# Optimization experiments

Hardware: AMD Instinct MI355X
Metric: run time of the kernel (lower is better)

## Reference

```python
import jax, jax.numpy as jnp
import numpy as np

EPS_SIGMA = 1e-6
EPS_NORM = 1e-6


def _filters(mu_x, mu_y, sigma_x, sigma_y, W, H):
    # squash params as in forward(): tanh for means, sigmoid for sigmas
    mu_x = jnp.tanh(mu_x)
    mu_y = jnp.tanh(mu_y)
    sx = jnp.exp(1.5 - 2.0 * jax.nn.sigmoid(sigma_x))  # [N]
    sy = jnp.exp(1.5 - 2.0 * jax.nn.sigmoid(sigma_y))
    # Sigma is diagonal, so its inverse is elementwise reciprocal
    inv_x = 1.0 / (sx ** 2 + EPS_SIGMA)  # [N]
    inv_y = 1.0 / (sy ** 2 + EPS_SIGMA)
    mux = (W - 1) * ((mu_x + 1.0) / 2.0)  # [N], pixel-space mean along width
    muy = (H - 1) * ((mu_y + 1.0) / 2.0)
    xs = jnp.arange(W, dtype=jnp.float32)
    ys = jnp.arange(H, dtype=jnp.float32)
    dx = xs[None, :, None] - mux[:, None, None]  # [N,W,1]
    dy = ys[None, None, :] - muy[:, None, None]  # [N,1,H]
    quad = dx ** 2 * inv_x[:, None, None] + dy ** 2 * inv_y[:, None, None]  # [N,W,H]
    f = jnp.exp(-0.5 * quad)
    return f / (jnp.sum(f, axis=(1, 2), keepdims=True) + EPS_NORM)  # [N,W,H]


def setup_inputs() -> dict:
    key = jax.random.key(0)
    k1, k2, k3, k4, k5 = jax.random.split(key, 5)
    B, C, T, W, H, N = 8, 1024, 64, 14, 14, 3
    video = jax.random.normal(k1, (B, C, T, W, H), dtype=jnp.float32)
    mu_x = 0.5 * jax.random.normal(k2, (N,), dtype=jnp.float32)
    mu_y = 0.5 * jax.random.normal(k3, (N,), dtype=jnp.float32)
    sigma_x = 1e-4 * jax.random.normal(k4, (N,), dtype=jnp.float32)
    sigma_y = 1e-4 * jax.random.normal(k5, (N,), dtype=jnp.float32)
    return {"video": video, "mu_x": mu_x, "mu_y": mu_y,
            "sigma_x": sigma_x, "sigma_y": sigma_y}


def reference(video, mu_x, mu_y, sigma_x, sigma_y):
    B, C, T, W, H = video.shape
    f = _filters(mu_x, mu_y, sigma_x, sigma_y, W, H)  # [N,W,H]
    N = f.shape[0]
    # weighted spatial sum, then mean over time; avoids the Ni-repeated video
    o = jnp.einsum('bctwh,nwh->bcn', video, f) / T  # [B,C,N]
    return o.reshape(B, C * N)
```

## Files before the change

kernel.cpp:

```cpp
#include <hip/hip_runtime.h>
#include <math.h>

#define B_  8
#define C_  1024
#define T_  64
#define W_  14
#define H_  14
#define N_  3
#define WH  (W_ * H_)
#define WH4 (WH / 4)

__global__ void attn_pool_kernel(const float* __restrict__ video,
                                 const float* __restrict__ mu_x,
                                 const float* __restrict__ mu_y,
                                 const float* __restrict__ sigma_x,
                                 const float* __restrict__ sigma_y,
                                 float* __restrict__ out)
{
    const int wave = threadIdx.x >> 6;
    const int lane = threadIdx.x & 63;
    const int bc   = blockIdx.x * 4 + wave;

    float fv[N_][4];
#pragma unroll
    for (int n = 0; n < N_; ++n)
#pragma unroll
        for (int j = 0; j < 4; ++j) fv[n][j] = 0.0f;

    if (lane < WH4) {
#pragma unroll
        for (int n = 0; n < N_; ++n) {
            const float mux  = 6.5f * (tanhf(mu_x[n]) + 1.0f);
            const float muy  = 6.5f * (tanhf(mu_y[n]) + 1.0f);
            const float sgx  = 1.0f / (1.0f + expf(-sigma_x[n]));
            const float sgy  = 1.0f / (1.0f + expf(-sigma_y[n]));
            const float invx = 1.0f / (expf(3.0f - 4.0f * sgx) + 1e-6f);
            const float invy = 1.0f / (expf(3.0f - 4.0f * sgy) + 1e-6f);
#pragma unroll
            for (int j = 0; j < 4; ++j) {
                const int   wh = 4 * lane + j;
                const int   w  = wh / H_;
                const int   h  = wh - w * H_;
                const float dx = (float)w - mux;
                const float dy = (float)h - muy;
                fv[n][j] = expf(-0.5f * (dx * dx * invx + dy * dy * invy));
            }
        }
    }
#pragma unroll
    for (int n = 0; n < N_; ++n) {
        float s = fv[n][0] + fv[n][1] + fv[n][2] + fv[n][3];
#pragma unroll
        for (int off = 32; off > 0; off >>= 1) s += __shfl_xor(s, off);
        const float norm = 1.0f / (s + 1e-6f);
#pragma unroll
        for (int j = 0; j < 4; ++j) fv[n][j] *= norm;
    }

    const float4* v4 = (const float4*)(video + (size_t)bc * (size_t)(T_ * WH));
    float a0 = 0.0f, a1 = 0.0f, a2 = 0.0f;
    if (lane < WH4) {
#pragma unroll 8
        for (int t = 0; t < T_; ++t) {
            const float4 v = v4[t * WH4 + lane];
            a0 += v.x * fv[0][0] + v.y * fv[0][1] + v.z * fv[0][2] + v.w * fv[0][3];
            a1 += v.x * fv[1][0] + v.y * fv[1][1] + v.z * fv[1][2] + v.w * fv[1][3];
            a2 += v.x * fv[2][0] + v.y * fv[2][1] + v.z * fv[2][2] + v.w * fv[2][3];
        }
    }
#pragma unroll
    for (int off = 32; off > 0; off >>= 1) {
        a0 += __shfl_xor(a0, off);
        a1 += __shfl_xor(a1, off);
        a2 += __shfl_xor(a2, off);
    }
    if (lane == 0) {
        float* o = out + (size_t)bc * N_;
        o[0] = a0 * (1.0f / T_);
        o[1] = a1 * (1.0f / T_);
        o[2] = a2 * (1.0f / T_);
    }
}

extern "C" void kernel_launch(void* const* d_in, const int* in_sizes, int n_in,
                              void* d_out, int out_size, void* d_ws, size_t ws_size,
                              hipStream_t stream) {
    const float* video   = (const float*)d_in[0];
    const float* mu_x    = (const float*)d_in[1];
    const float* mu_y    = (const float*)d_in[2];
    const float* sigma_x = (const float*)d_in[3];
    const float* sigma_y = (const float*)d_in[4];
    float* out = (float*)d_out;

    const int waves  = B_ * C_;
    const int blocks = waves / 4;
    attn_pool_kernel<<<blocks, 256, 0, stream>>>(video, mu_x, mu_y,
                                                 sigma_x, sigma_y, out);
}
```

Baseline: 535.7 us.

## Compute filters once per block in LDS and use all 64 lanes for loads

```diff
diff --git a/kernel.cpp b/kernel.cpp
--- a/kernel.cpp
+++ b/kernel.cpp
@@ -7,35 +7,35 @@
 #define W_  14
 #define H_  14
 #define N_  3
-#define WH  (W_ * H_)
-#define WH4 (WH / 4)
+#define WH    (W_ * H_)
+#define WH4   (WH / 4)
+#define SLAB4 (T_ * WH4)
 
-__global__ void attn_pool_kernel(const float* __restrict__ video,
-                                 const float* __restrict__ mu_x,
-                                 const float* __restrict__ mu_y,
-                                 const float* __restrict__ sigma_x,
-                                 const float* __restrict__ sigma_y,
-                                 float* __restrict__ out)
+__global__ __launch_bounds__(256) void attn_pool_kernel(
+        const float* __restrict__ video,
+        const float* __restrict__ mu_x,
+        const float* __restrict__ mu_y,
+        const float* __restrict__ sigma_x,
+        const float* __restrict__ sigma_y,
+        float* __restrict__ out)
 {
+    __shared__ float4 fsh[N_][WH4];
+
     const int wave = threadIdx.x >> 6;
     const int lane = threadIdx.x & 63;
     const int bc   = blockIdx.x * 4 + wave;
 
-    float fv[N_][4];
-#pragma unroll
-    for (int n = 0; n < N_; ++n)
-#pragma unroll
-        for (int j = 0; j < 4; ++j) fv[n][j] = 0.0f;
-
-    if (lane < WH4) {
-#pragma unroll
-        for (int n = 0; n < N_; ++n) {
+    if (wave < N_) {
+        const int n = wave;
+        float w0 = 0.0f, w1 = 0.0f, w2 = 0.0f, w3 = 0.0f;
+        if (lane < WH4) {
             const float mux  = 6.5f * (tanhf(mu_x[n]) + 1.0f);
             const float muy  = 6.5f * (tanhf(mu_y[n]) + 1.0f);
             const float sgx  = 1.0f / (1.0f + expf(-sigma_x[n]));
             const float sgy  = 1.0f / (1.0f + expf(-sigma_y[n]));
             const float invx = 1.0f / (expf(3.0f - 4.0f * sgx) + 1e-6f);
             const float invy = 1.0f / (expf(3.0f - 4.0f * sgy) + 1e-6f);
+            float wv[4];
 #pragma unroll
             for (int j = 0; j < 4; ++j) {
                 const int   wh = 4 * lane + j;
@@ -43,30 +43,33 @@
                 const int   h  = wh - w * H_;
                 const float dx = (float)w - mux;
                 const float dy = (float)h - muy;
-                fv[n][j] = expf(-0.5f * (dx * dx * invx + dy * dy * invy));
+                wv[j] = expf(-0.5f * (dx * dx * invx + dy * dy * invy));
             }
+            w0 = wv[0]; w1 = wv[1]; w2 = wv[2]; w3 = wv[3];
         }
-    }
-#pragma unroll
-    for (int n = 0; n < N_; ++n) {
-        float s = fv[n][0] + fv[n][1] + fv[n][2] + fv[n][3];
+        float s = w0 + w1 + w2 + w3;
 #pragma unroll
         for (int off = 32; off > 0; off >>= 1) s += __shfl_xor(s, off);
         const float norm = 1.0f / (s + 1e-6f);
-#pragma unroll
-        for (int j = 0; j < 4; ++j) fv[n][j] *= norm;
+        if (lane < WH4)
+            fsh[n][lane] = make_float4(w0 * norm, w1 * norm, w2 * norm, w3 * norm);
     }
+    __syncthreads();
 
-    const float4* v4 = (const float4*)(video + (size_t)bc * (size_t)(T_ * WH));
+    const float4* v4 = (const float4*)video + (size_t)bc * (size_t)SLAB4;
+    int r = (lane >= WH4) ? lane - WH4 : lane;
     float a0 = 0.0f, a1 = 0.0f, a2 = 0.0f;
-    if (lane < WH4) {
-#pragma unroll 8
-        for (int t = 0; t < T_; ++t) {
-            const float4 v = v4[t * WH4 + lane];
-            a0 += v.x * fv[0][0] + v.y * fv[0][1] + v.z * fv[0][2] + v.w * fv[0][3];
-            a1 += v.x * fv[1][0] + v.y * fv[1][1] + v.z * fv[1][2] + v.w * fv[1][3];
-            a2 += v.x * fv[2][0] + v.y * fv[2][1] + v.z * fv[2][2] + v.w * fv[2][3];
-        }
+#pragma unroll 7
+    for (int i = 0; i < WH4; ++i) {
+        const float4 v  = v4[i * 64 + lane];
+        const float4 f0 = fsh[0][r];
+        const float4 f1 = fsh[1][r];
+        const float4 f2 = fsh[2][r];
+        a0 += v.x * f0.x + v.y * f0.y + v.z * f0.z + v.w * f0.w;
+        a1 += v.x * f1.x + v.y * f1.y + v.z * f1.z + v.w * f1.w;
+        a2 += v.x * f2.x + v.y * f2.y + v.z * f2.z + v.w * f2.w;
+        r += 64 - WH4;
+        if (r >= WH4) r -= WH4;
     }
 #pragma unroll
     for (int off = 32; off > 0; off >>= 1) {
```

After: 533.6 us. No clear change (-0.4%).
